# Optimization experiments

Measured on AMD Instinct MI355X. Metric: run time of the kernel, lower is better.

Reference implementation:

```python
import jax, jax.numpy as jnp
import numpy as np

NTOKENS = 50257
EMB = 1024
N = 8192
K = 10            # noise_ratio
NORM_TERM = 9.0   # lnZ


def setup_inputs() -> dict:
    key = jax.random.key(0)
    k1, k2, k3, k4, k5, k6 = jax.random.split(key, 6)
    inp = jax.random.normal(k1, (N, EMB), dtype=jnp.float32)
    target = jax.random.randint(k2, (N,), 0, NTOKENS)
    noise_samples = jax.random.randint(k3, (N, K), 0, NTOKENS)
    # decoder params (nn.Linear(emb_size, ntokens)): weight (V, E), bias (V)
    bound = 1.0 / np.sqrt(EMB)
    weight = jax.random.uniform(k4, (NTOKENS, EMB), minval=-bound, maxval=bound, dtype=jnp.float32)
    bias = jax.random.uniform(k5, (NTOKENS,), minval=-bound, maxval=bound, dtype=jnp.float32)
    # noise distribution over the vocabulary (normalized)
    p = jax.random.uniform(k6, (NTOKENS,), minval=0.1, maxval=1.0, dtype=jnp.float32)
    noise = p / jnp.sum(p)
    return {"input": inp, "weight": weight, "bias": bias, "noise": noise,
            "target": target, "noise_samples": noise_samples}


def reference(input, weight, bias, noise, target, noise_samples):
    # indices per token: [target, noise_0..noise_{k-1}] -> (N, K+1)
    idx = jnp.concatenate([target[:, None], noise_samples], axis=1)
    w = weight[idx]                      # (N, K+1, E) gathered rows
    b = bias[idx]                        # (N, K+1)
    logits = jnp.einsum('ne,nke->nk', input, w) + b
    probs = jnp.exp(logits - NORM_TERM)  # unnormalized model probs
    data_prob = probs[:, 0]              # (N,)
    noise_in_data_probs = probs[:, 1:]   # (N, K)
    noise_probs = noise[noise_samples]   # (N, K)
    k = jnp.float32(K)
    rnn_loss = jnp.log(data_prob / (data_prob + k * noise[target]))
    noise_loss = jnp.sum(
        jnp.log(k * noise_probs / (noise_in_data_probs + k * noise_probs)), axis=1)
    loss = -jnp.sum(rnn_loss + noise_loss)
    return loss / N  # size_average=True
```

## Files before the change

### kernel.cpp

```cpp
#include <hip/hip_runtime.h>

#define N_TOK 8192
#define EMB 1024
#define KNOISE 10
#define NORM_TERM 9.0f

__global__ __launch_bounds__(256) void nce_token_kernel(
    const float* __restrict__ input,
    const float* __restrict__ weight,
    const float* __restrict__ bias,
    const float* __restrict__ noise,
    const int* __restrict__ target,
    const int* __restrict__ noise_samples,
    float* __restrict__ token_loss)
{
    __shared__ float4 s_in[EMB / 4];
    __shared__ float s_dot[16];

    const int n = blockIdx.x;
    const int tid = threadIdx.x;
    const int wave = tid >> 6;
    const int lane = tid & 63;

    s_in[tid] = reinterpret_cast<const float4*>(input + (size_t)n * EMB)[tid];
    __syncthreads();

    for (int k = wave; k < KNOISE + 1; k += 4) {
        const int row = (k == 0) ? target[n] : noise_samples[n * KNOISE + (k - 1)];
        const float4* wrow = reinterpret_cast<const float4*>(weight + (size_t)row * EMB);
        float acc = 0.f;
        #pragma unroll
        for (int j = 0; j < 4; ++j) {
            const float4 w4 = wrow[lane + 64 * j];
            const float4 i4 = s_in[lane + 64 * j];
            acc = fmaf(w4.x, i4.x, acc);
            acc = fmaf(w4.y, i4.y, acc);
            acc = fmaf(w4.z, i4.z, acc);
            acc = fmaf(w4.w, i4.w, acc);
        }
        #pragma unroll
        for (int off = 32; off > 0; off >>= 1)
            acc += __shfl_xor(acc, off, 64);
        if (lane == 0) s_dot[k] = acc + bias[row];
    }
    __syncthreads();

    if (tid == 0) {
        const int t = target[n];
        const float p0 = expf(s_dot[0] - NORM_TERM);
        const float kn0 = (float)KNOISE * noise[t];
        float loss = logf(p0 / (p0 + kn0));
        #pragma unroll
        for (int k = 0; k < KNOISE; ++k) {
            const int s = noise_samples[n * KNOISE + k];
            const float pk = expf(s_dot[k + 1] - NORM_TERM);
            const float kn = (float)KNOISE * noise[s];
            loss += logf(kn / (pk + kn));
        }
        token_loss[n] = loss;
    }
}

__global__ __launch_bounds__(256) void nce_reduce_kernel(
    const float* __restrict__ token_loss, float* __restrict__ out)
{
    __shared__ float s_part[4];
    float acc = 0.f;
    for (int i = threadIdx.x; i < N_TOK; i += 256)
        acc += token_loss[i];
    #pragma unroll
    for (int off = 32; off > 0; off >>= 1)
        acc += __shfl_xor(acc, off, 64);
    const int wave = threadIdx.x >> 6;
    const int lane = threadIdx.x & 63;
    if (lane == 0) s_part[wave] = acc;
    __syncthreads();
    if (threadIdx.x == 0) {
        const float total = s_part[0] + s_part[1] + s_part[2] + s_part[3];
        out[0] = -total / (float)N_TOK;
    }
}

extern "C" void kernel_launch(void* const* d_in, const int* in_sizes, int n_in,
                              void* d_out, int out_size, void* d_ws, size_t ws_size,
                              hipStream_t stream) {
    const float* input         = (const float*)d_in[0];
    const float* weight        = (const float*)d_in[1];
    const float* bias          = (const float*)d_in[2];
    const float* noise         = (const float*)d_in[3];
    const int*   target        = (const int*)d_in[4];
    const int*   noise_samples = (const int*)d_in[5];

    float* token_loss = (float*)d_ws;

    nce_token_kernel<<<N_TOK, 256, 0, stream>>>(
        input, weight, bias, noise, target, noise_samples, token_loss);
    nce_reduce_kernel<<<1, 256, 0, stream>>>(token_loss, (float*)d_out);
}
```

Before: 73.86 us.

## Bucket-sort gathered rows by vocab index before computing dot products

Replaces the per-token kernel with a pipeline: a histogram, scan and scatter bucket all (token, sample) items by weight-row range, then a dot kernel processes the items in sorted order with an XCD-style block swizzle, followed by a loss kernel and a final reduction. The intent is to make gathered weight-row accesses local in cache, raising L2 reuse of the 200MB weight table. In exchange it adds seven launches, atomics, and per-item reloads of input rows that were previously staged once in shared memory.

```diff
diff --git a/kernel.cpp b/kernel.cpp
--- a/kernel.cpp
+++ b/kernel.cpp
@@ -1,99 +1,167 @@
 #include <hip/hip_runtime.h>
 
-#define N_TOK 8192
+#define NTOK 8192
 #define EMB 1024
 #define KNOISE 10
+#define KP1 11
+#define M_ITEMS (NTOK * KP1)
+#define NVOCAB 50257
+#define BSHIFT 6
+#define NB ((NVOCAB + 63) >> 6)
 #define NORM_TERM 9.0f
 
-__global__ __launch_bounds__(256) void nce_token_kernel(
-    const float* __restrict__ input,
-    const float* __restrict__ weight,
-    const float* __restrict__ bias,
-    const float* __restrict__ noise,
-    const int* __restrict__ target,
-    const int* __restrict__ noise_samples,
-    float* __restrict__ token_loss)
-{
-    __shared__ float4 s_in[EMB / 4];
-    __shared__ float s_dot[16];
+#define OFF_HIST   0
+#define OFF_CURSOR 4096
+#define OFF_ROW    8192
+#define OFF_M      (OFF_ROW + M_ITEMS * 4)
+#define OFF_LOGIT  (OFF_M + M_ITEMS * 4)
+#define OFF_PART   (OFF_LOGIT + M_ITEMS * 4)
 
-    const int n = blockIdx.x;
-    const int tid = threadIdx.x;
-    const int wave = tid >> 6;
-    const int lane = tid & 63;
-
-    s_in[tid] = reinterpret_cast<const float4*>(input + (size_t)n * EMB)[tid];
-    __syncthreads();
-
-    for (int k = wave; k < KNOISE + 1; k += 4) {
-        const int row = (k == 0) ? target[n] : noise_samples[n * KNOISE + (k - 1)];
-        const float4* wrow = reinterpret_cast<const float4*>(weight + (size_t)row * EMB);
-        float acc = 0.f;
-        #pragma unroll
-        for (int j = 0; j < 4; ++j) {
-            const float4 w4 = wrow[lane + 64 * j];
-            const float4 i4 = s_in[lane + 64 * j];
-            acc = fmaf(w4.x, i4.x, acc);
-            acc = fmaf(w4.y, i4.y, acc);
-            acc = fmaf(w4.z, i4.z, acc);
-            acc = fmaf(w4.w, i4.w, acc);
-        }
-        #pragma unroll
-        for (int off = 32; off > 0; off >>= 1)
-            acc += __shfl_xor(acc, off, 64);
-        if (lane == 0) s_dot[k] = acc + bias[row];
-    }
-    __syncthreads();
-
-    if (tid == 0) {
-        const int t = target[n];
-        const float p0 = expf(s_dot[0] - NORM_TERM);
-        const float kn0 = (float)KNOISE * noise[t];
-        float loss = logf(p0 / (p0 + kn0));
-        #pragma unroll
-        for (int k = 0; k < KNOISE; ++k) {
-            const int s = noise_samples[n * KNOISE + k];
-            const float pk = expf(s_dot[k + 1] - NORM_TERM);
-            const float kn = (float)KNOISE * noise[s];
-            loss += logf(kn / (pk + kn));
-        }
-        token_loss[n] = loss;
-    }
+__device__ __forceinline__ int item_row(int m, const int* __restrict__ target,
+                                        const int* __restrict__ ns) {
+    const int n = (unsigned)m / KP1;
+    const int j = m - n * KP1;
+    return (j == 0) ? target[n] : ns[n * KNOISE + (j - 1)];
 }
 
-__global__ __launch_bounds__(256) void nce_reduce_kernel(
-    const float* __restrict__ token_loss, float* __restrict__ out)
+__global__ __launch_bounds__(1024) void zero_hist_kernel(int* __restrict__ hist) {
+    if (threadIdx.x < NB) hist[threadIdx.x] = 0;
+}
+
+__global__ __launch_bounds__(256) void hist_kernel(
+    const int* __restrict__ target, const int* __restrict__ ns,
+    int* __restrict__ hist)
 {
-    __shared__ float s_part[4];
+    const int m = blockIdx.x * 256 + threadIdx.x;
+    const int row = item_row(m, target, ns);
+    atomicAdd(&hist[row >> BSHIFT], 1);
+}
+
+__global__ __launch_bounds__(1024) void scan_kernel(
+    const int* __restrict__ hist, int* __restrict__ cursor)
+{
+    __shared__ int s[1024];
+    const int t = threadIdx.x;
+    const int v = (t < NB) ? hist[t] : 0;
+    s[t] = v;
+    __syncthreads();
+    #pragma unroll
+    for (int off = 1; off < 1024; off <<= 1) {
+        int u = (t >= off) ? s[t - off] : 0;
+        __syncthreads();
+        s[t] += u;
+        __syncthreads();
+    }
+    if (t < NB) cursor[t] = s[t] - v;
+}
+
+__global__ __launch_bounds__(256) void scatter_kernel(
+    const int* __restrict__ target, const int* __restrict__ ns,
+    int* __restrict__ cursor, int* __restrict__ sorted_row, int* __restrict__ sorted_m)
+{
+    const int m = blockIdx.x * 256 + threadIdx.x;
+    const int row = item_row(m, target, ns);
+    const int pos = atomicAdd(&cursor[row >> BSHIFT], 1);
+    sorted_row[pos] = row;
+    sorted_m[pos] = m;
+}
+
+__global__ __launch_bounds__(256) void dot_kernel(
+    const float* __restrict__ input, const float* __restrict__ weight,
+    const float* __restrict__ bias,
+    const int* __restrict__ sorted_row, const int* __restrict__ sorted_m,
+    float* __restrict__ logits)
+{
+    const int nblk = M_ITEMS / 4;
+    const int bid = blockIdx.x;
+    const int swz = (bid & 7) * (nblk >> 3) + (bid >> 3);
+    const int item = swz * 4 + (threadIdx.x >> 6);
+    const int lane = threadIdx.x & 63;
+
+    const int row = sorted_row[item];
+    const int m = sorted_m[item];
+    const int n = (unsigned)m / KP1;
+
+    const float4* wr = reinterpret_cast<const float4*>(weight + (size_t)row * EMB);
+    const float4* xr = reinterpret_cast<const float4*>(input + (size_t)n * EMB);
     float acc = 0.f;
-    for (int i = threadIdx.x; i < N_TOK; i += 256)
-        acc += token_loss[i];
+    #pragma unroll
+    for (int j = 0; j < 4; ++j) {
+        const float4 w4 = wr[lane + 64 * j];
+        const float4 x4 = xr[lane + 64 * j];
+        acc = fmaf(w4.x, x4.x, acc);
+        acc = fmaf(w4.y, x4.y, acc);
+        acc = fmaf(w4.z, x4.z, acc);
+        acc = fmaf(w4.w, x4.w, acc);
+    }
     #pragma unroll
     for (int off = 32; off > 0; off >>= 1)
         acc += __shfl_xor(acc, off, 64);
-    const int wave = threadIdx.x >> 6;
-    const int lane = threadIdx.x & 63;
-    if (lane == 0) s_part[wave] = acc;
+    if (lane == 0) logits[m] = acc + bias[row];
+}
+
+__global__ __launch_bounds__(256) void loss_kernel(
+    const float* __restrict__ logits, const float* __restrict__ noise,
+    const int* __restrict__ target, const int* __restrict__ ns,
+    float* __restrict__ partials)
+{
+    const int n = blockIdx.x * 256 + threadIdx.x;
+    const float* lg = logits + n * KP1;
+    const int t = target[n];
+    const float p0 = expf(lg[0] - NORM_TERM);
+    const float kn0 = (float)KNOISE * noise[t];
+    float loss = logf(p0 / (p0 + kn0));
+    #pragma unroll
+    for (int k = 0; k < KNOISE; ++k) {
+        const int s = ns[n * KNOISE + k];
+        const float pk = expf(lg[k + 1] - NORM_TERM);
+        const float kn = (float)KNOISE * noise[s];
+        loss += logf(kn / (pk + kn));
+    }
+    __shared__ float red[256];
+    red[threadIdx.x] = loss;
     __syncthreads();
+    #pragma unroll
+    for (int off = 128; off > 0; off >>= 1) {
+        if (threadIdx.x < off) red[threadIdx.x] += red[threadIdx.x + off];
+        __syncthreads();
+    }
+    if (threadIdx.x == 0) partials[blockIdx.x] = red[0];
+}
+
+__global__ __launch_bounds__(64) void final_kernel(
+    const float* __restrict__ partials, float* __restrict__ out)
+{
     if (threadIdx.x == 0) {
-        const float total = s_part[0] + s_part[1] + s_part[2] + s_part[3];
-        out[0] = -total / (float)N_TOK;
+        float s = 0.f;
+        for (int i = 0; i < 32; ++i) s += partials[i];
+        out[0] = -s / (float)NTOK;
     }
 }
 
 extern "C" void kernel_launch(void* const* d_in, const int* in_sizes, int n_in,
                               void* d_out, int out_size, void* d_ws, size_t ws_size,
                               hipStream_t stream) {
-    const float* input         = (const float*)d_in[0];
-    const float* weight        = (const float*)d_in[1];
-    const float* bias          = (const float*)d_in[2];
-    const float* noise         = (const float*)d_in[3];
-    const int*   target        = (const int*)d_in[4];
-    const int*   noise_samples = (const int*)d_in[5];
+    const float* input  = (const float*)d_in[0];
+    const float* weight = (const float*)d_in[1];
+    const float* bias   = (const float*)d_in[2];
+    const float* noise  = (const float*)d_in[3];
+    const int* target   = (const int*)d_in[4];
+    const int* ns       = (const int*)d_in[5];
 
-    float* token_loss = (float*)d_ws;
+    char* ws = (char*)d_ws;
+    int* hist       = (int*)(ws + OFF_HIST);
+    int* cursor     = (int*)(ws + OFF_CURSOR);
+    int* sorted_row = (int*)(ws + OFF_ROW);
+    int* sorted_m   = (int*)(ws + OFF_M);
+    float* logits   = (float*)(ws + OFF_LOGIT);
+    float* partials = (float*)(ws + OFF_PART);
 
-    nce_token_kernel<<<N_TOK, 256, 0, stream>>>(
-        input, weight, bias, noise, target, noise_samples, token_loss);
-    nce_reduce_kernel<<<1, 256, 0, stream>>>(token_loss, (float*)d_out);
+    zero_hist_kernel<<<1, 1024, 0, stream>>>(hist);
+    hist_kernel<<<M_ITEMS / 256, 256, 0, stream>>>(target, ns, hist);
+    scan_kernel<<<1, 1024, 0, stream>>>(hist, cursor);
+    scatter_kernel<<<M_ITEMS / 256, 256, 0, stream>>>(target, ns, cursor, sorted_row, sorted_m);
+    dot_kernel<<<M_ITEMS / 4, 256, 0, stream>>>(input, weight, bias, sorted_row, sorted_m, logits);
+    loss_kernel<<<NTOK / 256, 256, 0, stream>>>(logits, noise, target, ns, partials);
+    final_kernel<<<1, 64, 0, stream>>>(partials, (float*)d_out);
 }
```

Measured after the change: 135.7 us. +83.7%, slower.
